# Performance work log

Measured on AMD Instinct MI355X. Metric: run time of the kernel, lower is better.

Reference implementation:

```python
import jax, jax.numpy as jnp
import numpy as np

# ---- dopri5 (RK45) tableau ----
C2, C3, C4, C5 = 1/5, 3/10, 4/5, 8/9
A21 = 1/5
A31, A32 = 3/40, 9/40
A41, A42, A43 = 44/45, -56/15, 32/9
A51, A52, A53, A54 = 19372/6561, -25360/2187, 64448/6561, -212/729
A61, A62, A63, A64, A65 = 9017/3168, -355/33, 46732/5247, 49/176, -5103/18656
B1, B3, B4, B5, B6 = 35/384, 500/1113, 125/192, -2187/6784, 11/84
# error coefficients = b(5th) - b(4th)
E1, E3, E4, E5, E6, E7 = 71/57600, -71/16695, 71/1920, -17253/339200, 22/525, -1/40

N_STEPS = 24          # fixed scan length for the adaptive loop (jit-friendly)
RTOL = ATOL = 1e-3    # tolerance from init_kwargs
DT0 = 0.1             # initial step size


def conv_time(t, x, w, b, padding):
    # append time as an extra channel, then NCHW conv
    t_img = jnp.full_like(x[:, :1], t)
    xt = jnp.concatenate([t_img, x], axis=1)
    y = jax.lax.conv_general_dilated(xt, w, (1, 1), padding,
                                     dimension_numbers=('NCHW', 'OIHW', 'NCHW'))
    return y + b[None, :, None, None]


def ode_func(t, x, w1, b1, w2, b2, w3, b3):
    h = jax.nn.relu(conv_time(t, x, w1, b1, [(0, 0), (0, 0)]))
    h = jax.nn.relu(conv_time(t, h, w2, b2, [(1, 1), (1, 1)]))
    return conv_time(t, h, w3, b3, [(0, 0), (0, 0)])


def dopri5_step(f, t, y, dt):
    k1 = f(t, y)
    k2 = f(t + dt * C2, y + dt * (A21 * k1))
    k3 = f(t + dt * C3, y + dt * (A31 * k1 + A32 * k2))
    k4 = f(t + dt * C4, y + dt * (A41 * k1 + A42 * k2 + A43 * k3))
    k5 = f(t + dt * C5, y + dt * (A51 * k1 + A52 * k2 + A53 * k3 + A54 * k4))
    k6 = f(t + dt, y + dt * (A61 * k1 + A62 * k2 + A63 * k3 + A64 * k4 + A65 * k5))
    y5 = y + dt * (B1 * k1 + B3 * k3 + B4 * k4 + B5 * k5 + B6 * k6)
    k7 = f(t + dt, y5)  # FSAL stage, used for error estimate
    err = dt * (E1 * k1 + E3 * k3 + E4 * k4 + E5 * k5 + E6 * k6 + E7 * k7)
    return y5, err


def integrate(f, y0):
    """Adaptive dopri5 from t=0 to t=1 with fixed-length masked scan."""
    def step(carry, _):
        t, y, dt = carry
        dt_c = jnp.minimum(dt, 1.0 - t)
        y_new, err = dopri5_step(f, t, y, dt_c)
        tol = ATOL + RTOL * jnp.maximum(jnp.abs(y), jnp.abs(y_new))
        err_norm = jnp.sqrt(jnp.mean((err / tol) ** 2))
        done = t >= 1.0 - 1e-7
        adv = (err_norm <= 1.0) & (~done)
        t_n = jnp.where(adv, t + dt_c, t)
        y_n = jnp.where(adv, y_new, y)
        safe = jnp.maximum(err_norm, 1e-10)
        factor = jnp.clip(0.9 * safe ** (-0.2), 0.2, 10.0)
        dt_n = jnp.where(done, dt, dt_c * factor)
        return (t_n, y_n, dt_n), None

    step = jax.checkpoint(step)
    (t, y, dt), _ = jax.lax.scan(step,
                                 (jnp.float32(0.0), y0, jnp.float32(DT0)),
                                 None, length=N_STEPS)
    return y


def setup_inputs() -> dict:
    key = jax.random.key(0)
    ks = jax.random.split(key, 9)
    B, Cin, H, W = 64, 3, 32, 32
    AUG, NF = 5, 64
    CH = Cin + AUG  # 8
    x = jax.random.normal(ks[0], (B, Cin, H, W), dtype=jnp.float32)
    def wgt(k, shape):
        fan_in = shape[1] * shape[2] * shape[3]
        return jax.random.normal(k, shape, dtype=jnp.float32) / np.sqrt(fan_in).astype(np.float32)
    w1 = wgt(ks[1], (NF, CH + 1, 1, 1)); b1 = jnp.zeros((NF,), jnp.float32)
    w2 = wgt(ks[2], (NF, NF + 1, 3, 3)); b2 = jnp.zeros((NF,), jnp.float32)
    w3 = wgt(ks[3], (CH, NF + 1, 1, 1)); b3 = jnp.zeros((CH,), jnp.float32)
    flat = CH * H * W  # 8192
    wl = jax.random.normal(ks[4], (10, flat), dtype=jnp.float32) / np.sqrt(flat).astype(np.float32)
    bl = jnp.zeros((10,), jnp.float32)
    return {"x": x, "w1": w1, "b1": b1, "w2": w2, "b2": b2,
            "w3": w3, "b3": b3, "wl": wl, "bl": bl}


def reference(x, w1, b1, w2, b2, w3, b3, wl, bl):
    B, C, H, W = x.shape
    AUG = w3.shape[0] - C  # augmented channels
    aug = jnp.zeros((B, AUG, H, W), dtype=x.dtype)
    y0 = jnp.concatenate([x, aug], axis=1)
    f = lambda t, y: ode_func(t, y, w1, b1, w2, b2, w3, b3)
    yT = integrate(f, y0)                    # state at t = 1
    out = yT.reshape(B, -1) @ wl.T + bl      # final linear head
    return out
```

## Files before the change

### kernel.cpp

```cpp
#include <hip/hip_runtime.h>
#include <math.h>

namespace {
constexpr int BN = 64;
constexpr int HW = 1024;
constexpr int NS = BN*8*HW;

constexpr float C2f = 0.2f, C3f = 0.3f, C4f = 0.8f, C5f = (float)(8.0/9.0);
constexpr float A21 = 0.2f;
constexpr float A31 = (float)(3.0/40.0),  A32 = (float)(9.0/40.0);
constexpr float A41 = (float)(44.0/45.0), A42 = (float)(-56.0/15.0), A43 = (float)(32.0/9.0);
constexpr float A51 = (float)(19372.0/6561.0), A52 = (float)(-25360.0/2187.0),
                A53 = (float)(64448.0/6561.0), A54 = (float)(-212.0/729.0);
constexpr float A61 = (float)(9017.0/3168.0), A62 = (float)(-355.0/33.0),
                A63 = (float)(46732.0/5247.0), A64 = (float)(49.0/176.0),
                A65 = (float)(-5103.0/18656.0);
constexpr float B1c = (float)(35.0/384.0), B3c = (float)(500.0/1113.0),
                B4c = (float)(125.0/192.0), B5c = (float)(-2187.0/6784.0),
                B6c = (float)(11.0/84.0);
constexpr float E1c = (float)(71.0/57600.0), E3c = (float)(-71.0/16695.0),
                E4c = (float)(71.0/1920.0), E5c = (float)(-17253.0/339200.0),
                E6c = (float)(22.0/525.0),  E7c = (float)(-1.0/40.0);
constexpr float RTOL = 1e-3f, ATOL = 1e-3f;

constexpr size_t OFF_PART = 0;
constexpr size_t OFF_FLAG = 1024;
constexpr size_t OFF_CNT  = 1536;
constexpr size_t OFF_TSUM = 1600;
constexpr size_t OFF_W2P  = 2176;
constexpr size_t OFF_Y    = 20608;
constexpr size_t OFF_Y5   = OFF_Y  + (size_t)NS;
constexpr size_t OFF_K    = OFF_Y5 + (size_t)NS;
constexpr size_t OFF_WPK  = OFF_K + (size_t)7*NS;
constexpr size_t OFF_FT   = OFF_WPK + 1152;
constexpr size_t OFF_FB   = OFF_FT + 512;

constexpr int ACT_STRIDE = 272;
constexpr int H2_STRIDE  = 144;
}

__constant__ float g_cf[6][5] = {
    {A21, 0, 0, 0, 0},
    {A31, A32, 0, 0, 0},
    {A41, A42, A43, 0, 0},
    {A51, A52, A53, A54, 0},
    {A61, A62, A63, A64, A65},
    {0, 0, 0, 0, 0}};
__constant__ float g_ct[6] = {C2f, C3f, C4f, C5f, 1.0f, 1.0f};

typedef _Float16 hfrag8 __attribute__((ext_vector_type(8)));
typedef float f32x16 __attribute__((ext_vector_type(16)));

union HU { hfrag8 h; unsigned u[4]; uint4 v; };

__device__ __forceinline__ float ld_sysf(const float* p) {
    return __hip_atomic_load(p, __ATOMIC_RELAXED, __HIP_MEMORY_SCOPE_SYSTEM);
}
__device__ __forceinline__ float2 ld_sysf2(const float* p) {
    union { unsigned long long u; float2 f; } c;
    c.u = __hip_atomic_load((const unsigned long long*)p, __ATOMIC_RELAXED,
                            __HIP_MEMORY_SCOPE_SYSTEM);
    return c.f;
}
__device__ __forceinline__ void st_sysf(float* p, float v) {
    __hip_atomic_store(p, v, __ATOMIC_RELAXED, __HIP_MEMORY_SCOPE_SYSTEM);
}
__device__ __forceinline__ void st_sysf2(float* p, float a, float b) {
    union { unsigned long long u; float2 f; } c;
    c.f = make_float2(a, b);
    __hip_atomic_store((unsigned long long*)p, c.u, __ATOMIC_RELAXED,
                       __HIP_MEMORY_SCOPE_SYSTEM);
}

__device__ __forceinline__ void ld8(const float* p, float* v, bool sys) {
    if (sys) {
        #pragma unroll
        for (int h = 0; h < 4; h++) {
            float2 t = ld_sysf2(p + 2*h);
            v[2*h] = t.x; v[2*h+1] = t.y;
        }
    } else {
        float4 a = *(const float4*)p;
        float4 b = *(const float4*)(p + 4);
        v[0]=a.x; v[1]=a.y; v[2]=a.z; v[3]=a.w;
        v[4]=b.x; v[5]=b.y; v[6]=b.z; v[7]=b.w;
    }
}
__device__ __forceinline__ void st8(float* p, const float* v, bool sys) {
    if (sys) {
        st_sysf2(p,     v[0], v[1]);
        st_sysf2(p + 2, v[2], v[3]);
        st_sysf2(p + 4, v[4], v[5]);
        st_sysf2(p + 6, v[6], v[7]);
    } else {
        *(float4*)p       = make_float4(v[0], v[1], v[2], v[3]);
        *(float4*)(p + 4) = make_float4(v[4], v[5], v[6], v[7]);
    }
}

__global__ __launch_bounds__(256)
void k_init(const float* __restrict__ x, float* __restrict__ y,
            int* __restrict__ flags, int* __restrict__ flagT,
            int* __restrict__ flagB)
{
    int idx = blockIdx.x*256 + threadIdx.x;
    int b = idx >> 13, px = (idx >> 3) & 1023, c = idx & 7;
    y[idx] = (c < 3) ? x[(size_t)(b*3 + c)*1024 + px] : 0.0f;
    if (idx < 512) { flags[idx] = 0; flagT[idx] = 0; flagB[idx] = 0; }
}

__global__ __launch_bounds__(256)
void k_prepack(const float* __restrict__ w1, const float* __restrict__ w2,
               const float* __restrict__ w3, _Float16* __restrict__ w2p,
               float* __restrict__ tsum, float* __restrict__ wpk)
{
    int gid = blockIdx.x*256 + threadIdx.x;
    if (gid < 36864) {
        int j    = gid & 7;
        int lane = (gid >> 3) & 63;
        int nt   = (gid >> 9) & 1;
        int ks   = (gid >> 10) & 3;
        int tap  = gid >> 12;
        int oc = nt*32 + (lane & 31);
        int kpos = ks*16 + (lane >> 5)*8 + j;
        int oct = kpos >> 5, q2b = (kpos >> 4) & 1, rr = kpos & 15;
        int ic = oct*32 + (rr & 3) + (q2b << 2) + ((rr >> 2) << 3);
        w2p[gid] = (_Float16)w2[oc*585 + (1 + ic)*9 + tap];
    }
    if (gid < 576) {
        int oc = gid & 63, combo = gid >> 6;
        int rcase = combo / 3, ccase = combo % 3;
        float s = 0.0f;
        for (int kh = 0; kh < 3; kh++) {
            if ((rcase == 1 && kh == 0) || (rcase == 2 && kh == 2)) continue;
            for (int kw = 0; kw < 3; kw++) {
                if ((ccase == 1 && kw == 0) || (ccase == 2 && kw == 2)) continue;
                s += w2[oc*585 + kh*3 + kw];
            }
        }
        tsum[gid] = s;
    }
    if (gid < 512) wpk[gid] = w1[(gid & 63)*9 + 1 + (gid >> 6)];
    if (gid < 64)  wpk[512 + gid] = w1[gid*9];
    if (gid < 512) wpk[576 + gid] = w3[(gid & 7)*65 + 1 + (gid >> 3)];
    if (gid < 8)   wpk[1088 + gid] = w3[gid*65];
}

__global__ void __launch_bounds__(256, 2)
k_ode(const float* __restrict__ b1, const float* __restrict__ b2,
      const float* __restrict__ b3, const _Float16* __restrict__ w2p,
      const float* __restrict__ tsumg, const float* __restrict__ wpk,
      const float* __restrict__ wl, const float* __restrict__ bl,
      float* __restrict__ ybuf, float* __restrict__ y5buf,
      float* __restrict__ kb, float* __restrict__ part,
      int* __restrict__ flags, int* __restrict__ flagT,
      int* __restrict__ flagB, float* __restrict__ out)
{
    __shared__ __align__(16) unsigned char s_pool[192*ACT_STRIDE];
    __shared__ __align__(16) unsigned char s_h2[128*H2_STRIDE];
    __shared__ float s_tsum[576];
    __shared__ float s_b2v[64], s_b1v[64], s_w10v[64];
    __shared__ float s_w30v[8], s_b3v[8];
    __shared__ float s_red[8];

    const int tid = threadIdx.x;
    const int nblk = gridDim.x;
    const int lane = tid & 63;
    const int m32 = lane & 31, q2 = lane >> 5;
    const int rp = tid >> 7;
    const int np = (tid >> 6) & 1;
    const int wid = tid >> 6;
    const bool lz32 = (lane == 32);
    const bool lz31 = (lane == 31);

    if (tid < 64) {
        s_b2v[tid] = b2[tid];
        s_b1v[tid] = b1[tid];
        s_w10v[tid] = wpk[512 + tid];
    }
    if (tid < 8) { s_w30v[tid] = wpk[1088 + tid]; s_b3v[tid] = b3[tid]; }
    for (int i = tid; i < 576; i += 256) s_tsum[i] = tsumg[i];
    __syncthreads();

    hfrag8 w1lo[2], w1hi[2];
    #pragma unroll
    for (int oct = 0; oct < 2; oct++)
        #pragma unroll
        for (int j = 0; j < 8; j++) {
            _Float16 wv = (_Float16)wpk[j*64 + oct*32 + m32];
            w1lo[oct][j] = q2 ? (_Float16)0.0f : wv;
            w1hi[oct][j] = q2 ? wv : (_Float16)0.0f;
        }
    hfrag8 w3f[4];
    #pragma unroll
    for (int kst = 0; kst < 4; kst++)
        #pragma unroll
        for (int j = 0; j < 8; j++) {
            int kpos = kst*16 + q2*8 + j;
            int oct = kpos >> 5, q2b = (kpos >> 4) & 1, rr = kpos & 15;
            int ch = oct*32 + (rr & 3) + (q2b << 2) + ((rr >> 2) << 3);
            w3f[kst][j] = (m32 < 8) ? (_Float16)wpk[576 + ch*8 + m32]
                                    : (_Float16)0.0f;
        }

    float t = 0.0f, dt = 0.1f;
    float* ya = ybuf; float* yb = y5buf;
    float* ka = kb;  float* kg = kb + 6*(size_t)NS;

    auto wait_all = [&](int target) {
        for (;;) {
            bool ok = (__hip_atomic_load(&flags[tid], __ATOMIC_RELAXED,
                           __HIP_MEMORY_SCOPE_SYSTEM) >= target)
                   && (__hip_atomic_load(&flags[tid + 256], __ATOMIC_RELAXED,
                           __HIP_MEMORY_SCOPE_SYSTEM) >= target);
            if (__syncthreads_and((int)ok)) break;
            __builtin_amdgcn_s_sleep(2);
        }
    };

    auto eval = [&](const float* src, int nc, const float* cf, float ctv,
                    float* kout, int mode, int gev, float* partp) {
        float dtc = fminf(dt, 1.0f - t);
        float ts  = t + ctv*dtc;

        for (int tile = blockIdx.x; tile < 512; tile += nblk) {
            int b = tile >> 3, rg = tile & 7;

            auto zload = [&](int lr) {
                HU pz; pz.v = make_uint4(0u,0u,0u,0u);
                int r = rg*4 - 1 + lr;
                if ((unsigned)lr < 6u && (unsigned)r < 32u) {
                    bool nbr = (lr == 0) | (lr == 5);
                    int px = (r << 5) + m32;
                    size_t pb8 = ((size_t)(b << 10) + px) << 3;
                    float kv[5][8], sv[8];
                    if (nbr) {
                        #pragma unroll
                        for (int j = 0; j < 5; j++) if (j < nc) {
                            const float* kp = (j == 0 ? ka : kb + (size_t)j*NS) + pb8;
                            #pragma unroll
                            for (int h = 0; h < 4; h++) {
                                float2 t2 = ld_sysf2(kp + 2*h);
                                kv[j][2*h] = t2.x; kv[j][2*h+1] = t2.y;
                            }
                        }
                        #pragma unroll
                        for (int h = 0; h < 4; h++) {
                            float2 t2 = ld_sysf2(src + pb8 + 2*h);
                            sv[2*h] = t2.x; sv[2*h+1] = t2.y;
                        }
                    } else {
                        #pragma unroll
                        for (int j = 0; j < 5; j++) if (j < nc) {
                            const float* kp = (j == 0 ? ka : kb + (size_t)j*NS) + pb8;
                            float4 a4 = *(const float4*)kp;
                            float4 b4 = *(const float4*)(kp + 4);
                            kv[j][0]=a4.x; kv[j][1]=a4.y; kv[j][2]=a4.z; kv[j][3]=a4.w;
                            kv[j][4]=b4.x; kv[j][5]=b4.y; kv[j][6]=b4.z; kv[j][7]=b4.w;
                        }
                        float4 a4 = *(const float4*)(src + pb8);
                        float4 b4 = *(const float4*)(src + pb8 + 4);
                        sv[0]=a4.x; sv[1]=a4.y; sv[2]=a4.z; sv[3]=a4.w;
                        sv[4]=b4.x; sv[5]=b4.y; sv[6]=b4.z; sv[7]=b4.w;
                    }
                    float s[8] = {0,0,0,0,0,0,0,0};
                    #pragma unroll
                    for (int j = 0; j < 5; j++) if (j < nc) {
                        float a = cf[j];
                        #pragma unroll
                        for (int c = 0; c < 8; c++) s[c] = fmaf(a, kv[j][c], s[c]);
                    }
                    #pragma unroll
                    for (int c = 0; c < 8; c++)
                        pz.h[c] = (_Float16)(sv[c] + dtc*s[c]);
                }
                return pz;
            };

            HU pz;
            if (q2 == 0) pz = zload(wid + 1);
            if (gev > 1 && q2 == 1 && (wid == 0 || wid == 3)) {
                bool need = (wid == 0) ? (rg > 0) : (rg < 7);
                if (need) {
                    const int* fp = (wid == 0) ? &flagB[tile-1] : &flagT[tile+1];
                    while (__hip_atomic_load(fp, __ATOMIC_RELAXED,
                                             __HIP_MEMORY_SCOPE_SYSTEM) < gev-1)
                        __builtin_amdgcn_s_sleep(1);
                }
            }
            if (q2 == 1) pz = zload((wid == 0) ? 0 : ((wid == 3) ? 5 : -1));

            auto wr_act = [&](int lr, const f32x16& a1, int oct, bool valid) {
                unsigned words[8];
                #pragma unroll
                for (int pr = 0; pr < 8; pr++) {
                    int r0 = 2*pr;
                    int oc0 = oct*32 + (r0 & 3) + 8*(r0 >> 2) + 4*q2;
                    float v0 = valid ? fmaxf(a1[r0]   + ts*s_w10v[oc0]
                                             + s_b1v[oc0],   0.0f) : 0.0f;
                    float v1 = valid ? fmaxf(a1[r0+1] + ts*s_w10v[oc0+1]
                                             + s_b1v[oc0+1], 0.0f) : 0.0f;
                    union { _Float16 h[2]; unsigned u; } pk;
                    pk.h[0] = (_Float16)v0; pk.h[1] = (_Float16)v1;
                    words[pr] = pk.u;
                }
                unsigned char* basep = s_pool + (size_t)(lr*32 + m32)*ACT_STRIDE
                                       + oct*64 + q2*32;
                *(uint4*)basep        = make_uint4(words[0],words[1],words[2],words[3]);
                *(uint4*)(basep + 16) = make_uint4(words[4],words[5],words[6],words[7]);
            };
            {
                f32x16 zz = (f32x16)(0.0f);
                f32x16 c0 = __builtin_amdgcn_mfma_f32_32x32x16_f16(w1lo[0], pz.h, zz, 0,0,0);
                f32x16 c1 = __builtin_amdgcn_mfma_f32_32x32x16_f16(w1lo[1], pz.h, zz, 0,0,0);
                wr_act(wid + 1, c0, 0, true);
                wr_act(wid + 1, c1, 1, true);
                if (wid == 0 || wid == 3) {
                    int lrh = (wid == 0) ? 0 : 5;
                    bool vh = (unsigned)(rg*4 - 1 + lrh) < 32u;
                    f32x16 d0 = __builtin_amdgcn_mfma_f32_32x32x16_f16(w1hi[0], pz.h, zz, 0,0,0);
                    f32x16 d1 = __builtin_amdgcn_mfma_f32_32x32x16_f16(w1hi[1], pz.h, zz, 0,0,0);
                    wr_act(lrh, d0, 0, vh);
                    wr_act(lrh, d1, 1, vh);
                }
            }
            __syncthreads();

            f32x16 acc2[2];
            acc2[0] = (f32x16)(0.0f);
            acc2[1] = (f32x16)(0.0f);
            {
                const unsigned char* actb = (const unsigned char*)s_pool;
                #pragma unroll 1
                for (int ks = 0; ks < 4; ks++) {
                    HU fc[4], d0[4], d2[4];
                    #pragma unroll
                    for (int l = 0; l < 4; l++) {
                        const unsigned char* p = actb
                            + (size_t)((rp*2 + l)*32 + m32)*ACT_STRIDE
                            + ks*32 + q2*16;
                        fc[l].v = *(const uint4*)p;
                    }
                    #pragma unroll
                    for (int l = 0; l < 4; l++) {
                        #pragma unroll
                        for (int i = 0; i < 4; i++) {
                            unsigned s0 = (unsigned)__builtin_amdgcn_update_dpp(
                                0, (int)fc[l].u[i], 0x138, 0xF, 0xF, true);
                            d0[l].u[i] = lz32 ? 0u : s0;
                            unsigned s2 = (unsigned)__builtin_amdgcn_update_dpp(
                                0, (int)fc[l].u[i], 0x130, 0xF, 0xF, true);
                            d2[l].u[i] = lz31 ? 0u : s2;
                        }
                    }
                    #pragma unroll
                    for (int kh = 0; kh < 3; kh++) {
                        #pragma unroll
                        for (int kw = 0; kw < 3; kw++) {
                            int tap = kh*3 + kw;
                            hfrag8 aw = *(const hfrag8*)
                                (w2p + (size_t)((tap*4 + ks)*2 + np)*512 + lane*8);
                            #pragma unroll
                            for (int ri = 0; ri < 2; ri++) {
                                int l = ri + kh;
                                hfrag8 bf = (kw == 0) ? d0[l].h
                                          : ((kw == 1) ? fc[l].h : d2[l].h);
                                acc2[ri] = __builtin_amdgcn_mfma_f32_32x32x16_f16(
                                    aw, bf, acc2[ri], 0, 0, 0);
                            }
                        }
                    }
                }
            }

            {
                int ccase = (m32 == 0) ? 1 : ((m32 == 31) ? 2 : 0);
                #pragma unroll
                for (int ri = 0; ri < 2; ri++) {
                    int pg = rp*2 + ri;
                    int r_out = rg*4 + pg;
                    int rcase = (r_out == 0) ? 1 : ((r_out == 31) ? 2 : 0);
                    const float* tsb = &s_tsum[(rcase*3 + ccase)*64];
                    int px = pg*32 + m32;
                    unsigned words[8];
                    #pragma unroll
                    for (int pr = 0; pr < 8; pr++) {
                        int r0 = 2*pr;
                        int oc0 = np*32 + (r0 & 3) + 8*(r0 >> 2) + 4*q2;
                        float v0 = fmaxf(acc2[ri][r0]   + ts*tsb[oc0]
                                         + s_b2v[oc0],   0.0f);
                        float v1 = fmaxf(acc2[ri][r0+1] + ts*tsb[oc0+1]
                                         + s_b2v[oc0+1], 0.0f);
                        union { _Float16 h[2]; unsigned u; } pk;
                        pk.h[0] = (_Float16)v0; pk.h[1] = (_Float16)v1;
                        words[pr] = pk.u;
                    }
                    unsigned char* basep = s_h2 + (size_t)px*H2_STRIDE
                                           + np*64 + q2*32;
                    *(uint4*)basep        = make_uint4(words[0],words[1],words[2],words[3]);
                    *(uint4*)(basep + 16) = make_uint4(words[4],words[5],words[6],words[7]);
                }
            }
            __syncthreads();

            float ls = 0.0f;
            {
                f32x16 a3a = (f32x16)(0.0f);
                #pragma unroll
                for (int kst = 0; kst < 4; kst++) {
                    HU f;
                    const unsigned char* p = s_h2
                        + (size_t)(wid*32 + m32)*H2_STRIDE + kst*32 + q2*16;
                    f.v = *(const uint4*)p;
                    a3a = __builtin_amdgcn_mfma_f32_32x32x16_f16(
                        w3f[kst], f.h, a3a, 0, 0, 0);
                }
                float a3[8];
                #pragma unroll
                for (int r = 0; r < 4; r++) {
                    float own = a3a[r];
                    float oth = __shfl(own, lane ^ 32, 64);
                    a3[r]     = q2 ? oth : own;
                    a3[4 + r] = q2 ? own : oth;
                }
                if (q2 == 0) {
                    #pragma unroll
                    for (int c = 0; c < 8; c++)
                        a3[c] += fmaf(ts, s_w30v[c], s_b3v[c]);
                    bool sysrow = (wid == 0) | (wid == 3);
                    int px = rg*128 + wid*32 + m32;
                    size_t pb8 = ((size_t)(b << 10) + px) << 3;
                    st8(kout + pb8, a3, sysrow);
                    if (mode == 1) {
                        float kv1[8], kv3[8], kv4[8], kv5[8], yv[8], r8[8];
                        ld8(ka + pb8, kv1, false);
                        ld8(kb + 2*(size_t)NS + pb8, kv3, false);
                        ld8(kb + 3*(size_t)NS + pb8, kv4, false);
                        ld8(kb + 4*(size_t)NS + pb8, kv5, false);
                        ld8(ya + pb8, yv, false);
                        #pragma unroll
                        for (int c = 0; c < 8; c++)
                            r8[c] = yv[c] + dtc*(B1c*kv1[c] + B3c*kv3[c]
                                    + B4c*kv4[c] + B5c*kv5[c] + B6c*a3[c]);
                        st8(yb + pb8, r8, sysrow);
                    } else if (mode == 2) {
                        float kv1[8], kv3[8], kv4[8], kv5[8], kv6[8], yv[8], y5v[8];
                        ld8(ka + pb8, kv1, false);
                        ld8(kb + 2*(size_t)NS + pb8, kv3, false);
                        ld8(kb + 3*(size_t)NS + pb8, kv4, false);
                        ld8(kb + 4*(size_t)NS + pb8, kv5, false);
                        ld8(kb + 5*(size_t)NS + pb8, kv6, false);
                        ld8(ya + pb8, yv, false);
                        ld8(yb + pb8, y5v, false);
                        #pragma unroll
                        for (int c = 0; c < 8; c++) {
                            float e = dtc*(E1c*kv1[c] + E3c*kv3[c] + E4c*kv4[c]
                                           + E5c*kv5[c] + E6c*kv6[c] + E7c*a3[c]);
                            float tol = ATOL + RTOL*fmaxf(fabsf(yv[c]), fabsf(y5v[c]));
                            float rr = e / tol;
                            ls += rr*rr;
                        }
                    }
                }
            }
            asm volatile("s_waitcnt vmcnt(0)" ::: "memory");
            if (lane == 0 && wid == 0)
                __hip_atomic_store(&flagT[tile], gev, __ATOMIC_RELAXED,
                                   __HIP_MEMORY_SCOPE_SYSTEM);
            if (lane == 0 && wid == 3)
                __hip_atomic_store(&flagB[tile], gev, __ATOMIC_RELAXED,
                                   __HIP_MEMORY_SCOPE_SYSTEM);
            if (mode == 2) {
                float v = ls;
                #pragma unroll
                for (int off = 1; off < 64; off <<= 1)
                    v += __shfl_xor(v, off, 64);
                if (lane == 0) s_red[wid] = v;
                __syncthreads();
                if (tid == 0) {
                    st_sysf(&partp[tile],
                            s_red[0] + s_red[1] + s_red[2] + s_red[3]);
                    asm volatile("s_waitcnt vmcnt(0)" ::: "memory");
                    __hip_atomic_store(&flags[tile], gev, __ATOMIC_RELAXED,
                                       __HIP_MEMORY_SCOPE_SYSTEM);
                }
            }
        }
    };

    int gev = 1;
    eval(ya, 0, g_cf[5], 0.0f, ka, 0, gev, part);
    gev++;

    for (int st = 0; st < 24; st++) {
        if (t >= 1.0f - 1e-7f) break;
        float* partp = part + (size_t)(st & 1)*512;
        for (int e = 0; e < 6; e++) {
            int nc = (e < 5) ? e + 1 : 0;
            const float* src = (e == 5) ? yb : ya;
            float* kout = (e < 5) ? kb + (size_t)(e + 1)*NS : kg;
            int mode = (e == 4) ? 1 : ((e == 5) ? 2 : 0);
            eval(src, nc, g_cf[e], g_ct[e], kout, mode, gev, partp);
            gev++;
        }
        wait_all(gev - 1);
        float v = ld_sysf(&partp[tid]) + ld_sysf(&partp[tid + 256]);
        #pragma unroll
        for (int off = 1; off < 64; off <<= 1)
            v += __shfl_xor(v, off, 64);
        if (lane == 0) s_red[wid] = v;
        __syncthreads();
        float red0 = s_red[0] + s_red[1] + s_red[2] + s_red[3];
        float err_norm = sqrtf(red0 / (float)NS);
        float dtc = fminf(dt, 1.0f - t);
        bool adv = (err_norm <= 1.0f);
        if (adv) {
            t = t + dtc;
            float* tmp = ya; ya = yb; yb = tmp;
            tmp = ka; ka = kg; kg = tmp;
        }
        float safe = fmaxf(err_norm, 1e-10f);
        float factor = fminf(fmaxf(0.9f*powf(safe, -0.2f), 0.2f), 10.0f);
        dt = dtc*factor;
    }

    for (int tile = blockIdx.x; tile < 512; tile += nblk) {
        int b = tile >> 3, rg = tile & 7;
        if (tid < 128) {
            int lrow = tid >> 5;
            if (lrow == 1 || lrow == 2) {
                int px = rg*128 + tid;
                float* yp = ya + (((size_t)(b << 10) + px) << 3);
                float4 v0 = *(const float4*)yp;
                float4 v1 = *(const float4*)(yp + 4);
                st_sysf2(yp,     v0.x, v0.y);
                st_sysf2(yp + 2, v0.z, v0.w);
                st_sysf2(yp + 4, v1.x, v1.y);
                st_sysf2(yp + 6, v1.z, v1.w);
            }
        }
    }
    __syncthreads();
    for (int tile = blockIdx.x; tile < 512; tile += nblk)
        if (tid == 0)
            __hip_atomic_store(&flags[tile], gev, __ATOMIC_RELAXED,
                               __HIP_MEMORY_SCOPE_SYSTEM);
    wait_all(gev);

    for (int bh = blockIdx.x; bh < 64; bh += nblk) {
        float* s_hred = (float*)s_pool;
        float acc[10];
        #pragma unroll
        for (int m = 0; m < 10; m++) acc[m] = 0.0f;
        for (int px = tid; px < 1024; px += 256) {
            const float* yp = ya + (((size_t)(bh << 10) + px) << 3);
            float yv[8];
            #pragma unroll
            for (int h = 0; h < 4; h++) {
                float2 v = ld_sysf2(yp + 2*h);
                yv[2*h] = v.x; yv[2*h+1] = v.y;
            }
            #pragma unroll
            for (int c = 0; c < 8; c++) {
                float v = yv[c];
                #pragma unroll
                for (int m = 0; m < 10; m++)
                    acc[m] = fmaf(v, wl[(size_t)m*8192 + (c << 10) + px], acc[m]);
            }
        }
        #pragma unroll
        for (int m = 0; m < 10; m++) s_hred[m*256 + tid] = acc[m];
        __syncthreads();
        for (int sft = 128; sft > 0; sft >>= 1) {
            if (tid < sft) {
                #pragma unroll
                for (int m = 0; m < 10; m++)
                    s_hred[m*256 + tid] += s_hred[m*256 + tid + sft];
            }
            __syncthreads();
        }
        if (tid < 10) out[bh*10 + tid] = s_hred[tid*256] + bl[tid];
        __syncthreads();
    }
}

extern "C" void kernel_launch(void* const* d_in, const int* in_sizes, int n_in,
                              void* d_out, int out_size, void* d_ws, size_t ws_size,
                              hipStream_t stream)
{
    const float* x  = (const float*)d_in[0];
    const float* w1 = (const float*)d_in[1];
    const float* b1 = (const float*)d_in[2];
    const float* w2 = (const float*)d_in[3];
    const float* b2 = (const float*)d_in[4];
    const float* w3 = (const float*)d_in[5];
    const float* b3 = (const float*)d_in[6];
    const float* wl = (const float*)d_in[7];
    const float* bl = (const float*)d_in[8];
    float* out = (float*)d_out;

    float* F = (float*)d_ws;
    float* part = F + OFF_PART;
    int*   flags = (int*)(F + OFF_FLAG);
    float* tsum = F + OFF_TSUM;
    _Float16* w2p = (_Float16*)(F + OFF_W2P);
    float* y    = F + OFF_Y;
    float* y5   = F + OFF_Y5;
    float* kbp  = F + OFF_K;
    float* wpk  = F + OFF_WPK;
    int*   flagT = (int*)(F + OFF_FT);
    int*   flagB = (int*)(F + OFF_FB);

    k_init<<<NS/256, 256, 0, stream>>>(x, y, flags, flagT, flagB);
    k_prepack<<<144, 256, 0, stream>>>(w1, w2, w3, w2p, tsum, wpk);

    int maxb = 0;
    if (hipOccupancyMaxActiveBlocksPerMultiprocessor(&maxb,
            reinterpret_cast<const void*>(k_ode), 256, 0) != hipSuccess || maxb < 1)
        maxb = 1;
    int cus = 256;
    {
        int dev = 0;
        hipGetDevice(&dev);
        hipDeviceProp_t prop;
        if (hipGetDeviceProperties(&prop, dev) == hipSuccess && prop.multiProcessorCount > 0)
            cus = prop.multiProcessorCount;
    }
    long cap = (long)maxb * (long)cus;
    int gridn = (int)((cap < 512) ? cap : 512);
    if (gridn < 16) gridn = 16;

    k_ode<<<gridn, 256, 0, stream>>>(b1, b2, b3, w2p, tsum, wpk, wl, bl,
                                     y, y5, kbp, part, flags, flagT, flagB, out);
}
```

Before: 399.3 us.

## Keep RK stage values and state in registers when one tile per block

Adds a templated register-resident path. When the grid can hold all 512 tiles at once, each thread keeps its own pixels' k1..k7, y and y5 in registers. Only halo-edge rows are written to global memory for neighbouring tiles, which removes most of the global stores and reloads of stage values in the combine and error steps. This raises register pressure, which could hurt the 2-blocks-per-CU occupancy that the fast path depends on. If the grid cannot fit, it falls back to the old global-buffer kernel.

Result: slower. 503.8 us (+26.2%).

```diff
diff --git a/kernel.cpp b/kernel.cpp
--- a/kernel.cpp
+++ b/kernel.cpp
@@ -146,6 +146,7 @@
     if (gid < 8)   wpk[1088 + gid] = w3[gid*65];
 }
 
+template<bool REGK>
 __global__ void __launch_bounds__(256, 2)
 k_ode(const float* __restrict__ b1, const float* __restrict__ b2,
       const float* __restrict__ b3, const _Float16* __restrict__ w2p,
@@ -203,6 +204,15 @@
                                     : (_Float16)0.0f;
         }
 
+    float k1r[8], k2r[8], k3r[8], k4r[8], k5r[8], k6r[8], k7r[8], yr[8], y5r[8];
+    if constexpr (REGK) {
+        #pragma unroll
+        for (int c = 0; c < 8; c++) {
+            k1r[c]=0.f; k2r[c]=0.f; k3r[c]=0.f; k4r[c]=0.f; k5r[c]=0.f;
+            k6r[c]=0.f; k7r[c]=0.f; yr[c]=0.f; y5r[c]=0.f;
+        }
+    }
+
     float t = 0.0f, dt = 0.1f;
     float* ya = ybuf; float* yb = y5buf;
     float* ka = kb;  float* kg = kb + 6*(size_t)NS;
@@ -219,7 +229,8 @@
     };
 
     auto eval = [&](const float* src, int nc, const float* cf, float ctv,
-                    float* kout, int mode, int gev, float* partp) {
+                    float* kout, int mode, int gev, float* partp,
+                    int srcsel, int kslot) {
         float dtc = fminf(dt, 1.0f - t);
         float ts  = t + ctv*dtc;
 
@@ -278,7 +289,29 @@
             };
 
             HU pz;
-            if (q2 == 0) pz = zload(wid + 1);
+            if (q2 == 0) {
+                if constexpr (REGK) {
+                    if (srcsel == 2) {
+                        int px = ((rg*4 + wid) << 5) + m32;
+                        size_t pb8 = ((size_t)(b << 10) + px) << 3;
+                        ld8(src + pb8, yr, false);
+                        #pragma unroll
+                        for (int c = 0; c < 8; c++) pz.h[c] = (_Float16)yr[c];
+                    } else {
+                        float cf0 = cf[0], cf1 = cf[1], cf2 = cf[2],
+                              cf3 = cf[3], cf4 = cf[4];
+                        #pragma unroll
+                        for (int c = 0; c < 8; c++) {
+                            float s_ = cf0*k1r[c] + cf1*k2r[c] + cf2*k3r[c]
+                                     + cf3*k4r[c] + cf4*k5r[c];
+                            float base = (srcsel == 0) ? yr[c] : y5r[c];
+                            pz.h[c] = (_Float16)(base + dtc*s_);
+                        }
+                    }
+                } else {
+                    pz = zload(wid + 1);
+                }
+            }
             if (gev > 1 && q2 == 1 && (wid == 0 || wid == 3)) {
                 bool need = (wid == 0) ? (rg > 0) : (rg < 7);
                 if (need) {
@@ -427,38 +460,82 @@
                     #pragma unroll
                     for (int c = 0; c < 8; c++)
                         a3[c] += fmaf(ts, s_w30v[c], s_b3v[c]);
-                    bool sysrow = (wid == 0) | (wid == 3);
+                    bool edge = (wid == 0) | (wid == 3);
                     int px = rg*128 + wid*32 + m32;
                     size_t pb8 = ((size_t)(b << 10) + px) << 3;
-                    st8(kout + pb8, a3, sysrow);
-                    if (mode == 1) {
-                        float kv1[8], kv3[8], kv4[8], kv5[8], yv[8], r8[8];
-                        ld8(ka + pb8, kv1, false);
-                        ld8(kb + 2*(size_t)NS + pb8, kv3, false);
-                        ld8(kb + 3*(size_t)NS + pb8, kv4, false);
-                        ld8(kb + 4*(size_t)NS + pb8, kv5, false);
-                        ld8(ya + pb8, yv, false);
-                        #pragma unroll
-                        for (int c = 0; c < 8; c++)
-                            r8[c] = yv[c] + dtc*(B1c*kv1[c] + B3c*kv3[c]
-                                    + B4c*kv4[c] + B5c*kv5[c] + B6c*a3[c]);
-                        st8(yb + pb8, r8, sysrow);
-                    } else if (mode == 2) {
-                        float kv1[8], kv3[8], kv4[8], kv5[8], kv6[8], yv[8], y5v[8];
-                        ld8(ka + pb8, kv1, false);
-                        ld8(kb + 2*(size_t)NS + pb8, kv3, false);
-                        ld8(kb + 3*(size_t)NS + pb8, kv4, false);
-                        ld8(kb + 4*(size_t)NS + pb8, kv5, false);
-                        ld8(kb + 5*(size_t)NS + pb8, kv6, false);
-                        ld8(ya + pb8, yv, false);
-                        ld8(yb + pb8, y5v, false);
-                        #pragma unroll
-                        for (int c = 0; c < 8; c++) {
-                            float e = dtc*(E1c*kv1[c] + E3c*kv3[c] + E4c*kv4[c]
-                                           + E5c*kv5[c] + E6c*kv6[c] + E7c*a3[c]);
-                            float tol = ATOL + RTOL*fmaxf(fabsf(yv[c]), fabsf(y5v[c]));
-                            float rr = e / tol;
-                            ls += rr*rr;
+                    if constexpr (REGK) {
+                        if (edge) st8(kout + pb8, a3, true);
+                        if (mode == 1) {
+                            #pragma unroll
+                            for (int c = 0; c < 8; c++)
+                                y5r[c] = yr[c] + dtc*(B1c*k1r[c] + B3c*k3r[c]
+                                        + B4c*k4r[c] + B5c*k5r[c] + B6c*a3[c]);
+                            if (edge) st8(yb + pb8, y5r, true);
+                        } else if (mode == 2) {
+                            #pragma unroll
+                            for (int c = 0; c < 8; c++) {
+                                float e = dtc*(E1c*k1r[c] + E3c*k3r[c]
+                                        + E4c*k4r[c] + E5c*k5r[c]
+                                        + E6c*k6r[c] + E7c*a3[c]);
+                                float tol = ATOL + RTOL*fmaxf(fabsf(yr[c]),
+                                                              fabsf(y5r[c]));
+                                float rr = e / tol;
+                                ls += rr*rr;
+                            }
+                        }
+                        if (kslot == 1) {
+                            #pragma unroll
+                            for (int c = 0; c < 8; c++) k1r[c] = a3[c];
+                        } else if (kslot == 2) {
+                            #pragma unroll
+                            for (int c = 0; c < 8; c++) k2r[c] = a3[c];
+                        } else if (kslot == 3) {
+                            #pragma unroll
+                            for (int c = 0; c < 8; c++) k3r[c] = a3[c];
+                        } else if (kslot == 4) {
+                            #pragma unroll
+                            for (int c = 0; c < 8; c++) k4r[c] = a3[c];
+                        } else if (kslot == 5) {
+                            #pragma unroll
+                            for (int c = 0; c < 8; c++) k5r[c] = a3[c];
+                        } else if (kslot == 6) {
+                            #pragma unroll
+                            for (int c = 0; c < 8; c++) k6r[c] = a3[c];
+                        } else {
+                            #pragma unroll
+                            for (int c = 0; c < 8; c++) k7r[c] = a3[c];
+                        }
+                    } else {
+                        st8(kout + pb8, a3, edge);
+                        if (mode == 1) {
+                            float kv1[8], kv3[8], kv4[8], kv5[8], yv[8], r8[8];
+                            ld8(ka + pb8, kv1, false);
+                            ld8(kb + 2*(size_t)NS + pb8, kv3, false);
+                            ld8(kb + 3*(size_t)NS + pb8, kv4, false);
+                            ld8(kb + 4*(size_t)NS + pb8, kv5, false);
+                            ld8(ya + pb8, yv, false);
+                            #pragma unroll
+                            for (int c = 0; c < 8; c++)
+                                r8[c] = yv[c] + dtc*(B1c*kv1[c] + B3c*kv3[c]
+                                        + B4c*kv4[c] + B5c*kv5[c] + B6c*a3[c]);
+                            st8(yb + pb8, r8, edge);
+                        } else if (mode == 2) {
+                            float kv1[8], kv3[8], kv4[8], kv5[8], kv6[8], yv[8], y5v[8];
+                            ld8(ka + pb8, kv1, false);
+                            ld8(kb + 2*(size_t)NS + pb8, kv3, false);
+                            ld8(kb + 3*(size_t)NS + pb8, kv4, false);
+                            ld8(kb + 4*(size_t)NS + pb8, kv5, false);
+                            ld8(kb + 5*(size_t)NS + pb8, kv6, false);
+                            ld8(ya + pb8, yv, false);
+                            ld8(yb + pb8, y5v, false);
+                            #pragma unroll
+                            for (int c = 0; c < 8; c++) {
+                                float e = dtc*(E1c*kv1[c] + E3c*kv3[c] + E4c*kv4[c]
+                                               + E5c*kv5[c] + E6c*kv6[c] + E7c*a3[c]);
+                                float tol = ATOL + RTOL*fmaxf(fabsf(yv[c]), fabsf(y5v[c]));
+                                float rr = e / tol;
+                                ls += rr*rr;
+                            }
                         }
                     }
                 }
@@ -489,7 +566,7 @@
     };
 
     int gev = 1;
-    eval(ya, 0, g_cf[5], 0.0f, ka, 0, gev, part);
+    eval(ya, 0, g_cf[5], 0.0f, ka, 0, gev, part, 2, 1);
     gev++;
 
     for (int st = 0; st < 24; st++) {
@@ -500,7 +577,9 @@
             const float* src = (e == 5) ? yb : ya;
             float* kout = (e < 5) ? kb + (size_t)(e + 1)*NS : kg;
             int mode = (e == 4) ? 1 : ((e == 5) ? 2 : 0);
-            eval(src, nc, g_cf[e], g_ct[e], kout, mode, gev, partp);
+            int srcsel = (e == 5) ? 1 : 0;
+            eval(src, nc, g_cf[e], g_ct[e], kout, mode, gev, partp,
+                 srcsel, e + 2);
             gev++;
         }
         wait_all(gev - 1);
@@ -518,33 +597,57 @@
             t = t + dtc;
             float* tmp = ya; ya = yb; yb = tmp;
             tmp = ka; ka = kg; kg = tmp;
+            if constexpr (REGK) {
+                #pragma unroll
+                for (int c = 0; c < 8; c++) {
+                    yr[c]  = y5r[c];
+                    k1r[c] = k7r[c];
+                }
+            }
         }
         float safe = fmaxf(err_norm, 1e-10f);
         float factor = fminf(fmaxf(0.9f*powf(safe, -0.2f), 0.2f), 10.0f);
         dt = dtc*factor;
     }
 
-    for (int tile = blockIdx.x; tile < 512; tile += nblk) {
+    if constexpr (REGK) {
+        int tile = blockIdx.x;
         int b = tile >> 3, rg = tile & 7;
-        if (tid < 128) {
-            int lrow = tid >> 5;
-            if (lrow == 1 || lrow == 2) {
-                int px = rg*128 + tid;
-                float* yp = ya + (((size_t)(b << 10) + px) << 3);
-                float4 v0 = *(const float4*)yp;
-                float4 v1 = *(const float4*)(yp + 4);
-                st_sysf2(yp,     v0.x, v0.y);
-                st_sysf2(yp + 2, v0.z, v0.w);
-                st_sysf2(yp + 4, v1.x, v1.y);
-                st_sysf2(yp + 6, v1.z, v1.w);
-            }
-        }
-    }
-    __syncthreads();
-    for (int tile = blockIdx.x; tile < 512; tile += nblk)
+        if (q2 == 0) {
+            int px = rg*128 + wid*32 + m32;
+            float* yp = ya + (((size_t)(b << 10) + px) << 3);
+            st_sysf2(yp,     yr[0], yr[1]);
+            st_sysf2(yp + 2, yr[2], yr[3]);
+            st_sysf2(yp + 4, yr[4], yr[5]);
+            st_sysf2(yp + 6, yr[6], yr[7]);
+        }
+        __syncthreads();
         if (tid == 0)
             __hip_atomic_store(&flags[tile], gev, __ATOMIC_RELAXED,
                                __HIP_MEMORY_SCOPE_SYSTEM);
+    } else {
+        for (int tile = blockIdx.x; tile < 512; tile += nblk) {
+            int b = tile >> 3, rg = tile & 7;
+            if (tid < 128) {
+                int lrow = tid >> 5;
+                if (lrow == 1 || lrow == 2) {
+                    int px = rg*128 + tid;
+                    float* yp = ya + (((size_t)(b << 10) + px) << 3);
+                    float4 v0 = *(const float4*)yp;
+                    float4 v1 = *(const float4*)(yp + 4);
+                    st_sysf2(yp,     v0.x, v0.y);
+                    st_sysf2(yp + 2, v0.z, v0.w);
+                    st_sysf2(yp + 4, v1.x, v1.y);
+                    st_sysf2(yp + 6, v1.z, v1.w);
+                }
+            }
+        }
+        __syncthreads();
+        for (int tile = blockIdx.x; tile < 512; tile += nblk)
+            if (tid == 0)
+                __hip_atomic_store(&flags[tile], gev, __ATOMIC_RELAXED,
+                                   __HIP_MEMORY_SCOPE_SYSTEM);
+    }
     wait_all(gev);
 
     for (int bh = blockIdx.x; bh < 64; bh += nblk) {
@@ -614,10 +717,6 @@
     k_init<<<NS/256, 256, 0, stream>>>(x, y, flags, flagT, flagB);
     k_prepack<<<144, 256, 0, stream>>>(w1, w2, w3, w2p, tsum, wpk);
 
-    int maxb = 0;
-    if (hipOccupancyMaxActiveBlocksPerMultiprocessor(&maxb,
-            reinterpret_cast<const void*>(k_ode), 256, 0) != hipSuccess || maxb < 1)
-        maxb = 1;
     int cus = 256;
     {
         int dev = 0;
@@ -626,10 +725,26 @@
         if (hipGetDeviceProperties(&prop, dev) == hipSuccess && prop.multiProcessorCount > 0)
             cus = prop.multiProcessorCount;
     }
-    long cap = (long)maxb * (long)cus;
-    int gridn = (int)((cap < 512) ? cap : 512);
-    if (gridn < 16) gridn = 16;
-
-    k_ode<<<gridn, 256, 0, stream>>>(b1, b2, b3, w2p, tsum, wpk, wl, bl,
-                                     y, y5, kbp, part, flags, flagT, flagB, out);
-}
+
+    int maxbT = 0;
+    if (hipOccupancyMaxActiveBlocksPerMultiprocessor(&maxbT,
+            reinterpret_cast<const void*>(&k_ode<true>), 256, 0) != hipSuccess)
+        maxbT = 0;
+    if ((long)maxbT * (long)cus >= 512) {
+        k_ode<true><<<512, 256, 0, stream>>>(b1, b2, b3, w2p, tsum, wpk, wl, bl,
+                                             y, y5, kbp, part, flags, flagT,
+                                             flagB, out);
+    } else {
+        int maxbF = 0;
+        if (hipOccupancyMaxActiveBlocksPerMultiprocessor(&maxbF,
+                reinterpret_cast<const void*>(&k_ode<false>), 256, 0) != hipSuccess
+            || maxbF < 1)
+            maxbF = 1;
+        long cap = (long)maxbF * (long)cus;
+        int gridn = (int)((cap < 512) ? cap : 512);
+        if (gridn < 16) gridn = 16;
+        k_ode<false><<<gridn, 256, 0, stream>>>(b1, b2, b3, w2p, tsum, wpk, wl, bl,
+                                                y, y5, kbp, part, flags, flagT,
+                                                flagB, out);
+    }
+}
```

## Split conv2 into interior and halo phases to overlap neighbor waits

Applied to the files above, without the earlier changes.

Each tile's first-layer activations are now computed only for its own interior rows up front. The 3x3 conv runs on those interior rows before any halo data is needed. Meanwhile the edge waves wait on the neighbor-tile flags and issue the system-scope halo loads, then build the halo activation rows, and a second pass adds the halo-row taps. This is meant to hide inter-block flag spinning and slow halo loads behind MFMA work, at the cost of an extra block barrier and a templated duplicate of the conv loop.

New measurement: 716.7 us. 1.79x slower.

```diff
diff --git a/kernel.cpp b/kernel.cpp
--- a/kernel.cpp
+++ b/kernel.cpp
@@ -37,6 +37,8 @@
 
 constexpr int ACT_STRIDE = 272;
 constexpr int H2_STRIDE  = 144;
+
+template<int N> struct IC { static constexpr int value = N; };
 }
 
 __constant__ float g_cf[6][5] = {
@@ -226,70 +228,6 @@
         for (int tile = blockIdx.x; tile < 512; tile += nblk) {
             int b = tile >> 3, rg = tile & 7;
 
-            auto zload = [&](int lr) {
-                HU pz; pz.v = make_uint4(0u,0u,0u,0u);
-                int r = rg*4 - 1 + lr;
-                if ((unsigned)lr < 6u && (unsigned)r < 32u) {
-                    bool nbr = (lr == 0) | (lr == 5);
-                    int px = (r << 5) + m32;
-                    size_t pb8 = ((size_t)(b << 10) + px) << 3;
-                    float kv[5][8], sv[8];
-                    if (nbr) {
-                        #pragma unroll
-                        for (int j = 0; j < 5; j++) if (j < nc) {
-                            const float* kp = (j == 0 ? ka : kb + (size_t)j*NS) + pb8;
-                            #pragma unroll
-                            for (int h = 0; h < 4; h++) {
-                                float2 t2 = ld_sysf2(kp + 2*h);
-                                kv[j][2*h] = t2.x; kv[j][2*h+1] = t2.y;
-                            }
-                        }
-                        #pragma unroll
-                        for (int h = 0; h < 4; h++) {
-                            float2 t2 = ld_sysf2(src + pb8 + 2*h);
-                            sv[2*h] = t2.x; sv[2*h+1] = t2.y;
-                        }
-                    } else {
-                        #pragma unroll
-                        for (int j = 0; j < 5; j++) if (j < nc) {
-                            const float* kp = (j == 0 ? ka : kb + (size_t)j*NS) + pb8;
-                            float4 a4 = *(const float4*)kp;
-                            float4 b4 = *(const float4*)(kp + 4);
-                            kv[j][0]=a4.x; kv[j][1]=a4.y; kv[j][2]=a4.z; kv[j][3]=a4.w;
-                            kv[j][4]=b4.x; kv[j][5]=b4.y; kv[j][6]=b4.z; kv[j][7]=b4.w;
-                        }
-                        float4 a4 = *(const float4*)(src + pb8);
-                        float4 b4 = *(const float4*)(src + pb8 + 4);
-                        sv[0]=a4.x; sv[1]=a4.y; sv[2]=a4.z; sv[3]=a4.w;
-                        sv[4]=b4.x; sv[5]=b4.y; sv[6]=b4.z; sv[7]=b4.w;
-                    }
-                    float s[8] = {0,0,0,0,0,0,0,0};
-                    #pragma unroll
-                    for (int j = 0; j < 5; j++) if (j < nc) {
-                        float a = cf[j];
-                        #pragma unroll
-                        for (int c = 0; c < 8; c++) s[c] = fmaf(a, kv[j][c], s[c]);
-                    }
-                    #pragma unroll
-                    for (int c = 0; c < 8; c++)
-                        pz.h[c] = (_Float16)(sv[c] + dtc*s[c]);
-                }
-                return pz;
-            };
-
-            HU pz;
-            if (q2 == 0) pz = zload(wid + 1);
-            if (gev > 1 && q2 == 1 && (wid == 0 || wid == 3)) {
-                bool need = (wid == 0) ? (rg > 0) : (rg < 7);
-                if (need) {
-                    const int* fp = (wid == 0) ? &flagB[tile-1] : &flagT[tile+1];
-                    while (__hip_atomic_load(fp, __ATOMIC_RELAXED,
-                                             __HIP_MEMORY_SCOPE_SYSTEM) < gev-1)
-                        __builtin_amdgcn_s_sleep(1);
-                }
-            }
-            if (q2 == 1) pz = zload((wid == 0) ? 0 : ((wid == 3) ? 5 : -1));
-
             auto wr_act = [&](int lr, const f32x16& a1, int oct, bool valid) {
                 unsigned words[8];
                 #pragma unroll
@@ -309,48 +247,103 @@
                 *(uint4*)basep        = make_uint4(words[0],words[1],words[2],words[3]);
                 *(uint4*)(basep + 16) = make_uint4(words[4],words[5],words[6],words[7]);
             };
+
+            HU pz; pz.v = make_uint4(0u,0u,0u,0u);
+            if (q2 == 0) {
+                int px = (((rg*4 + wid)) << 5) + m32;
+                size_t pb8 = ((size_t)(b << 10) + px) << 3;
+                float kv[5][8], sv[8];
+                #pragma unroll
+                for (int j = 0; j < 5; j++) if (j < nc) {
+                    const float* kp = (j == 0 ? ka : kb + (size_t)j*NS) + pb8;
+                    float4 a4 = *(const float4*)kp;
+                    float4 b4 = *(const float4*)(kp + 4);
+                    kv[j][0]=a4.x; kv[j][1]=a4.y; kv[j][2]=a4.z; kv[j][3]=a4.w;
+                    kv[j][4]=b4.x; kv[j][5]=b4.y; kv[j][6]=b4.z; kv[j][7]=b4.w;
+                }
+                float4 a4 = *(const float4*)(src + pb8);
+                float4 b4 = *(const float4*)(src + pb8 + 4);
+                sv[0]=a4.x; sv[1]=a4.y; sv[2]=a4.z; sv[3]=a4.w;
+                sv[4]=b4.x; sv[5]=b4.y; sv[6]=b4.z; sv[7]=b4.w;
+                float s_[8] = {0,0,0,0,0,0,0,0};
+                #pragma unroll
+                for (int j = 0; j < 5; j++) if (j < nc) {
+                    float a = cf[j];
+                    #pragma unroll
+                    for (int c = 0; c < 8; c++) s_[c] = fmaf(a, kv[j][c], s_[c]);
+                }
+                #pragma unroll
+                for (int c = 0; c < 8; c++)
+                    pz.h[c] = (_Float16)(sv[c] + dtc*s_[c]);
+            }
             {
                 f32x16 zz = (f32x16)(0.0f);
                 f32x16 c0 = __builtin_amdgcn_mfma_f32_32x32x16_f16(w1lo[0], pz.h, zz, 0,0,0);
                 f32x16 c1 = __builtin_amdgcn_mfma_f32_32x32x16_f16(w1lo[1], pz.h, zz, 0,0,0);
                 wr_act(wid + 1, c0, 0, true);
                 wr_act(wid + 1, c1, 1, true);
-                if (wid == 0 || wid == 3) {
-                    int lrh = (wid == 0) ? 0 : 5;
-                    bool vh = (unsigned)(rg*4 - 1 + lrh) < 32u;
-                    f32x16 d0 = __builtin_amdgcn_mfma_f32_32x32x16_f16(w1hi[0], pz.h, zz, 0,0,0);
-                    f32x16 d1 = __builtin_amdgcn_mfma_f32_32x32x16_f16(w1hi[1], pz.h, zz, 0,0,0);
-                    wr_act(lrh, d0, 0, vh);
-                    wr_act(lrh, d1, 1, vh);
-                }
             }
             __syncthreads();
+
+            const bool edgew = (wid == 0) | (wid == 3);
+            const int lrh = (wid == 0) ? 0 : 5;
+            const int hr = rg*4 - 1 + lrh;
+            const bool hvalid = edgew && (q2 == 1) && ((unsigned)hr < 32u);
+            if (gev > 1 && edgew) {
+                bool need = (wid == 0) ? (rg > 0) : (rg < 7);
+                if (need) {
+                    const int* fp = (wid == 0) ? &flagB[tile-1] : &flagT[tile+1];
+                    while (__hip_atomic_load(fp, __ATOMIC_RELAXED,
+                                             __HIP_MEMORY_SCOPE_SYSTEM) < gev-1)
+                        __builtin_amdgcn_s_sleep(1);
+                }
+            }
+            float hkv[5][8], hsv[8];
+            if (hvalid) {
+                int px = (hr << 5) + m32;
+                size_t pb8 = ((size_t)(b << 10) + px) << 3;
+                #pragma unroll
+                for (int j = 0; j < 5; j++) if (j < nc) {
+                    const float* kp = (j == 0 ? ka : kb + (size_t)j*NS) + pb8;
+                    #pragma unroll
+                    for (int h = 0; h < 4; h++) {
+                        float2 t2 = ld_sysf2(kp + 2*h);
+                        hkv[j][2*h] = t2.x; hkv[j][2*h+1] = t2.y;
+                    }
+                }
+                #pragma unroll
+                for (int h = 0; h < 4; h++) {
+                    float2 t2 = ld_sysf2(src + pb8 + 2*h);
+                    hsv[2*h] = t2.x; hsv[2*h+1] = t2.y;
+                }
+            }
 
             f32x16 acc2[2];
             acc2[0] = (f32x16)(0.0f);
             acc2[1] = (f32x16)(0.0f);
-            {
-                const unsigned char* actb = (const unsigned char*)s_pool;
+            const unsigned char* actb = (const unsigned char*)s_pool;
+            auto part1 = [&](auto rpc) {
+                constexpr int RP = decltype(rpc)::value;
                 #pragma unroll 1
                 for (int ks = 0; ks < 4; ks++) {
-                    HU fc[4], d0[4], d2[4];
-                    #pragma unroll
-                    for (int l = 0; l < 4; l++) {
+                    HU fc[3], d0[3], d2[3];
+                    #pragma unroll
+                    for (int i = 0; i < 3; i++) {
+                        int lr = RP + 1 + i;
                         const unsigned char* p = actb
-                            + (size_t)((rp*2 + l)*32 + m32)*ACT_STRIDE
-                            + ks*32 + q2*16;
-                        fc[l].v = *(const uint4*)p;
-                    }
-                    #pragma unroll
-                    for (int l = 0; l < 4; l++) {
+                            + (size_t)(lr*32 + m32)*ACT_STRIDE + ks*32 + q2*16;
+                        fc[i].v = *(const uint4*)p;
+                    }
+                    #pragma unroll
+                    for (int i = 0; i < 3; i++) {
                         #pragma unroll
-                        for (int i = 0; i < 4; i++) {
+                        for (int u = 0; u < 4; u++) {
                             unsigned s0 = (unsigned)__builtin_amdgcn_update_dpp(
-                                0, (int)fc[l].u[i], 0x138, 0xF, 0xF, true);
-                            d0[l].u[i] = lz32 ? 0u : s0;
+                                0, (int)fc[i].u[u], 0x138, 0xF, 0xF, true);
+                            d0[i].u[u] = lz32 ? 0u : s0;
                             unsigned s2 = (unsigned)__builtin_amdgcn_update_dpp(
-                                0, (int)fc[l].u[i], 0x130, 0xF, 0xF, true);
-                            d2[l].u[i] = lz31 ? 0u : s2;
+                                0, (int)fc[i].u[u], 0x130, 0xF, 0xF, true);
+                            d2[i].u[u] = lz31 ? 0u : s2;
                         }
                     }
                     #pragma unroll
@@ -362,16 +355,76 @@
                                 (w2p + (size_t)((tap*4 + ks)*2 + np)*512 + lane*8);
                             #pragma unroll
                             for (int ri = 0; ri < 2; ri++) {
-                                int l = ri + kh;
-                                hfrag8 bf = (kw == 0) ? d0[l].h
-                                          : ((kw == 1) ? fc[l].h : d2[l].h);
+                                constexpr_int:;
+                                int lr = RP*2 + ri + kh;
+                                if (lr < 1 || lr > 4) continue;
+                                int i = RP + ri + kh - 1;
+                                hfrag8 bf = (kw == 0) ? d0[i].h
+                                          : ((kw == 1) ? fc[i].h : d2[i].h);
                                 acc2[ri] = __builtin_amdgcn_mfma_f32_32x32x16_f16(
                                     aw, bf, acc2[ri], 0, 0, 0);
                             }
                         }
                     }
                 }
-            }
+            };
+            if (rp == 0) part1(IC<0>{}); else part1(IC<1>{});
+
+            if (edgew) {
+                HU pzh; pzh.v = make_uint4(0u,0u,0u,0u);
+                if (hvalid) {
+                    float s_[8] = {0,0,0,0,0,0,0,0};
+                    #pragma unroll
+                    for (int j = 0; j < 5; j++) if (j < nc) {
+                        float a = cf[j];
+                        #pragma unroll
+                        for (int c = 0; c < 8; c++) s_[c] = fmaf(a, hkv[j][c], s_[c]);
+                    }
+                    #pragma unroll
+                    for (int c = 0; c < 8; c++)
+                        pzh.h[c] = (_Float16)(hsv[c] + dtc*s_[c]);
+                }
+                f32x16 zz = (f32x16)(0.0f);
+                f32x16 d0 = __builtin_amdgcn_mfma_f32_32x32x16_f16(w1hi[0], pzh.h, zz, 0,0,0);
+                f32x16 d1 = __builtin_amdgcn_mfma_f32_32x32x16_f16(w1hi[1], pzh.h, zz, 0,0,0);
+                bool vh = (unsigned)hr < 32u;
+                wr_act(lrh, d0, 0, vh);
+                wr_act(lrh, d1, 1, vh);
+            }
+            __syncthreads();
+
+            auto part2 = [&](auto rpc) {
+                constexpr int RP = decltype(rpc)::value;
+                constexpr int lr2 = (RP == 0) ? 0 : 5;
+                constexpr int kh2 = (RP == 0) ? 0 : 2;
+                constexpr int ri2 = (RP == 0) ? 0 : 1;
+                #pragma unroll 1
+                for (int ks = 0; ks < 4; ks++) {
+                    HU fc, d0, d2;
+                    const unsigned char* p = actb
+                        + (size_t)(lr2*32 + m32)*ACT_STRIDE + ks*32 + q2*16;
+                    fc.v = *(const uint4*)p;
+                    #pragma unroll
+                    for (int u = 0; u < 4; u++) {
+                        unsigned s0 = (unsigned)__builtin_amdgcn_update_dpp(
+                            0, (int)fc.u[u], 0x138, 0xF, 0xF, true);
+                        d0.u[u] = lz32 ? 0u : s0;
+                        unsigned s2 = (unsigned)__builtin_amdgcn_update_dpp(
+                            0, (int)fc.u[u], 0x130, 0xF, 0xF, true);
+                        d2.u[u] = lz31 ? 0u : s2;
+                    }
+                    #pragma unroll
+                    for (int kw = 0; kw < 3; kw++) {
+                        int tap = kh2*3 + kw;
+                        hfrag8 aw = *(const hfrag8*)
+                            (w2p + (size_t)((tap*4 + ks)*2 + np)*512 + lane*8);
+                        hfrag8 bf = (kw == 0) ? d0.h : ((kw == 1) ? fc.h : d2.h);
+                        acc2[ri2] = __builtin_amdgcn_mfma_f32_32x32x16_f16(
+                            aw, bf, acc2[ri2], 0, 0, 0);
+                    }
+                }
+            };
+            if (rp == 0) part2(IC<0>{}); else part2(IC<1>{});
 
             {
                 int ccase = (m32 == 0) ? 1 : ((m32 == 31) ? 2 : 0);
@@ -427,10 +480,10 @@
                     #pragma unroll
                     for (int c = 0; c < 8; c++)
                         a3[c] += fmaf(ts, s_w30v[c], s_b3v[c]);
-                    bool sysrow = (wid == 0) | (wid == 3);
+                    bool edge = (wid == 0) | (wid == 3);
                     int px = rg*128 + wid*32 + m32;
                     size_t pb8 = ((size_t)(b << 10) + px) << 3;
-                    st8(kout + pb8, a3, sysrow);
+                    st8(kout + pb8, a3, edge);
                     if (mode == 1) {
                         float kv1[8], kv3[8], kv4[8], kv5[8], yv[8], r8[8];
                         ld8(ka + pb8, kv1, false);
@@ -442,7 +495,7 @@
                         for (int c = 0; c < 8; c++)
                             r8[c] = yv[c] + dtc*(B1c*kv1[c] + B3c*kv3[c]
                                     + B4c*kv4[c] + B5c*kv5[c] + B6c*a3[c]);
-                        st8(yb + pb8, r8, sysrow);
+                        st8(yb + pb8, r8, edge);
                     } else if (mode == 2) {
                         float kv1[8], kv3[8], kv4[8], kv5[8], kv6[8], yv[8], y5v[8];
                         ld8(ka + pb8, kv1, false);
```
